# Kernel optimization log

Measured on AMD Instinct MI355X. Metric: run time of the kernel, lower is better.

The kernel has to match this reference:

```python
import jax, jax.numpy as jnp
import numpy as np

_K = 256  # d_model // 8


def setup_inputs() -> dict:
    key = jax.random.key(0)
    ks = jax.random.split(key, 7)
    B, T, D = 4, 4096, 2048
    x = jax.random.normal(ks[0], (B, T, D), jnp.float32)
    ema_mean = 0.1 * jax.random.normal(ks[1], (D,), jnp.float32)
    # ensure positive variance: ema_sq - ema_mean^2 in [0.5, 1.5]
    ema_sq = ema_mean ** 2 + 0.5 + jax.random.uniform(ks[2], (D,), jnp.float32)
    ema_out = jax.random.normal(ks[3], (D,), jnp.float32)
    log_tau = 0.1 * jax.random.normal(ks[4], (), jnp.float32)
    log_sigma_raw = 0.1 * jax.random.normal(ks[5], (), jnp.float32)
    log_w_raw = 0.1 * jax.random.normal(ks[6], (), jnp.float32)
    return {
        "x": x,
        "ema_mean": ema_mean,
        "ema_sq": ema_sq,
        "ema_out": ema_out,
        "log_tau": log_tau,
        "log_sigma_raw": log_sigma_raw,
        "log_w_raw": log_w_raw,
    }


def reference(x, ema_mean, ema_sq, ema_out, log_tau, log_sigma_raw, log_w_raw):
    tau = jnp.exp(log_tau)
    sigma = jax.nn.softplus(log_sigma_raw) + 0.01
    w = jax.nn.softplus(log_w_raw)

    out = jax.nn.gelu(x, approximate=False)  # F.gelu default = exact erf

    # z-score against EMA stats
    std = jnp.sqrt(jnp.clip(ema_sq - ema_mean ** 2, 1e-6, None))
    z = (x - ema_mean) / std

    # topk |z| over channel dim, gather z, mean of |z_topk|
    _, idx = jax.lax.top_k(jnp.abs(z), _K)          # idx: [B,T,K]
    z_topk = jnp.take_along_axis(z, idx, axis=-1)
    topk_mean = jnp.mean(jnp.abs(z_topk), axis=-1, keepdims=True)  # [B,T,1]
    surp = jnp.tanh(sigma * topk_mean)

    # cosine similarity of gelu output against EMA output direction
    ema_u = ema_out / (jnp.linalg.norm(ema_out) + 1e-8)
    out_n = out / jnp.maximum(
        jnp.linalg.norm(out, axis=-1, keepdims=True), 1e-12
    )  # F.normalize eps
    cos_out = jnp.sum(out_n * ema_u, axis=-1, keepdims=True)  # [B,T,1]

    gate = jnp.exp(-tau * cos_out) * (1.0 + w * surp)
    return out * gate
```

## Files before the change

kernel.cpp:

```cpp
#include <hip/hip_runtime.h>
#include <math.h>

#define D      2048
#define KSEL   256
#define NT     256
#define NBINS  256

typedef float vfloat4 __attribute__((ext_vector_type(4)));

__device__ __forceinline__ float fast_gelu(float x) {
    float x2 = x * x;
    float t  = fmaf(x2, -0.0713548162f, -1.5957691216f);
    float e  = __expf(x * t);
    return x * __builtin_amdgcn_rcpf(1.0f + e);
}

__global__ __launch_bounds__(NT) void prep_kernel(
    const float* __restrict__ ema_mean,
    const float* __restrict__ ema_sq,
    const float* __restrict__ ema_out,
    const float* __restrict__ p_log_tau,
    const float* __restrict__ p_log_sigma,
    const float* __restrict__ p_log_w,
    float* __restrict__ ws)
{
    __shared__ float red[4];
    const int tid = threadIdx.x;
    float ss = 0.f;
#pragma unroll
    for (int k = 0; k < D / NT; ++k) {
        int i = tid + k * NT;
        float m = ema_mean[i];
        float v = fmaxf(fmaf(-m, m, ema_sq[i]), 1e-6f);
        float inv = 32.0f * __builtin_amdgcn_rsqf(v);
        ws[i]     = inv;
        ws[D + i] = -m * inv;
        float e = ema_out[i];
        ss = fmaf(e, e, ss);
    }
#pragma unroll
    for (int o = 32; o > 0; o >>= 1) ss += __shfl_down(ss, o, 64);
    if ((tid & 63) == 0) red[tid >> 6] = ss;
    __syncthreads();
    float inv_nrm = 1.0f / (sqrtf(red[0] + red[1] + red[2] + red[3]) + 1e-8f);
#pragma unroll
    for (int k = 0; k < D / NT; ++k) {
        int i = tid + k * NT;
        ws[2 * D + i] = ema_out[i] * inv_nrm;
    }
    if (tid == 0) {
        ws[3 * D + 0] = __expf(p_log_tau[0]);
        ws[3 * D + 1] = __logf(1.0f + __expf(p_log_sigma[0])) + 0.01f;
        ws[3 * D + 2] = __logf(1.0f + __expf(p_log_w[0]));
    }
}

__global__ __launch_bounds__(NT) void row_kernel(
    const float* __restrict__ x,
    const float* __restrict__ ws,
    float* __restrict__ out)
{
    __shared__ int   hist[NBINS];
    __shared__ int   wsum[4];
    __shared__ float red[4][3];
    __shared__ int   bsel_sh, krem_sh;

    const int tid = threadIdx.x;
    const size_t rowoff = (size_t)blockIdx.x * D;
    const float* __restrict__ xr = x + rowoff;

    hist[tid] = 0;

    const float tau   = ws[3 * D + 0];
    const float sigma = ws[3 * D + 1];
    const float w     = ws[3 * D + 2];

    float4 xa = ((const float4*)xr)[tid];
    float4 xb = ((const float4*)xr)[tid + NT];
    float4 aa = ((const float4*)ws)[tid];
    float4 ab = ((const float4*)ws)[tid + NT];
    float4 ba = ((const float4*)(ws + D))[tid];
    float4 bb = ((const float4*)(ws + D))[tid + NT];
    float4 ua = ((const float4*)(ws + 2 * D))[tid];
    float4 ub = ((const float4*)(ws + 2 * D))[tid + NT];

    float xv[8] = {xa.x,xa.y,xa.z,xa.w, xb.x,xb.y,xb.z,xb.w};
    float avv[8] = {aa.x,aa.y,aa.z,aa.w, ab.x,ab.y,ab.z,ab.w};
    float bvv[8] = {ba.x,ba.y,ba.z,ba.w, bb.x,bb.y,bb.z,bb.w};
    float uv[8] = {ua.x,ua.y,ua.z,ua.w, ub.x,ub.y,ub.z,ub.w};

    float g[8], av[8];
    float dot = 0.f, nrm = 0.f;
#pragma unroll
    for (int j = 0; j < 8; ++j) {
        av[j] = fabsf(fmaf(xv[j], avv[j], bvv[j]));
        float gg = fast_gelu(xv[j]);
        g[j] = gg;
        dot = fmaf(gg, uv[j], dot);
        nrm = fmaf(gg, gg, nrm);
    }

    __syncthreads();
#pragma unroll
    for (int j = 0; j < 8; ++j) {
        int b = (int)fminf(av[j], 255.0f);
        atomicAdd(&hist[b], 1);
    }
    __syncthreads();

    {
        int bin = (NBINS - 1) - tid;
        int h = hist[bin];
        int p = h;
#pragma unroll
        for (int o = 1; o < 64; o <<= 1) {
            int t = __shfl_up(p, o, 64);
            if ((tid & 63) >= o) p += t;
        }
        if ((tid & 63) == 63) wsum[tid >> 6] = p;
        __syncthreads();
        int off = 0;
        for (int wv = 0; wv < (tid >> 6); ++wv) off += wsum[wv];
        int suf_incl = p + off;
        int suf_excl = suf_incl - h;
        if (suf_excl < KSEL && suf_incl >= KSEL) {
            bsel_sh = bin;
            krem_sh = KSEL - suf_excl;
        }
    }
    __syncthreads();

    const int   bsel = bsel_sh;
    const float hi  = (bsel == NBINS - 1) ? __builtin_inff() : (float)(bsel + 1);
    const float mid = (float)bsel + 0.5f;

    float s = 0.f;
#pragma unroll
    for (int j = 0; j < 8; ++j) {
        s += (av[j] >= hi) ? av[j] : 0.f;
    }

#pragma unroll
    for (int o = 32; o > 0; o >>= 1) {
        dot += __shfl_down(dot, o, 64);
        nrm += __shfl_down(nrm, o, 64);
        s   += __shfl_down(s,   o, 64);
    }
    const int wave = tid >> 6;
    if ((tid & 63) == 0) {
        red[wave][0] = dot; red[wave][1] = nrm; red[wave][2] = s;
    }
    __syncthreads();
    dot = red[0][0] + red[1][0] + red[2][0] + red[3][0];
    nrm = red[0][1] + red[1][1] + red[2][1] + red[3][1];
    s   = red[0][2] + red[1][2] + red[2][2] + red[3][2];

    const float topk_mean = (s + (float)krem_sh * mid) * (1.0f / (32.0f * KSEL));
    const float cosv = dot * __builtin_amdgcn_rsqf(fmaxf(nrm, 1e-24f));
    const float yt = sigma * topk_mean;
    const float et = __expf(-2.0f * yt);
    const float th = (1.0f - et) * __builtin_amdgcn_rcpf(1.0f + et);
    const float gate = __expf(-tau * cosv) * fmaf(w, th, 1.0f);

    vfloat4 oa, ob;
    oa.x = g[0]*gate; oa.y = g[1]*gate; oa.z = g[2]*gate; oa.w = g[3]*gate;
    ob.x = g[4]*gate; ob.y = g[5]*gate; ob.z = g[6]*gate; ob.w = g[7]*gate;
    vfloat4* outr = (vfloat4*)(out + rowoff);
    __builtin_nontemporal_store(oa, outr + tid);
    __builtin_nontemporal_store(ob, outr + tid + NT);
}

extern "C" void kernel_launch(void* const* d_in, const int* in_sizes, int n_in,
                              void* d_out, int out_size, void* d_ws, size_t ws_size,
                              hipStream_t stream) {
    (void)in_sizes; (void)n_in; (void)out_size; (void)ws_size;
    const float* x         = (const float*)d_in[0];
    const float* ema_mean  = (const float*)d_in[1];
    const float* ema_sq    = (const float*)d_in[2];
    const float* ema_out   = (const float*)d_in[3];
    const float* log_tau   = (const float*)d_in[4];
    const float* log_sigma = (const float*)d_in[5];
    const float* log_w     = (const float*)d_in[6];
    float* out = (float*)d_out;
    float* ws  = (float*)d_ws;

    prep_kernel<<<1, NT, 0, stream>>>(ema_mean, ema_sq, ema_out,
                                      log_tau, log_sigma, log_w, ws);
    const int rows = 4 * 4096;
    row_kernel<<<rows, NT, 0, stream>>>(x, ws, out);
}
```

Measured before the change: 51.71 us.

## Process two rows per 512-thread block and use packed float2 math

Each block now handles two rows with 512 threads, each half keeping its own histogram, scan and reduction buffers, which halves the grid size. The GELU, z-score and dot/norm accumulation are rewritten with two-wide float vectors so the compiler can emit packed FP32 instructions. Block-wide barriers now synchronise both rows together, so the two rows may stall each other. The row count is now taken from the input size.

```diff
diff --git a/kernel.cpp b/kernel.cpp
--- a/kernel.cpp
+++ b/kernel.cpp
@@ -6,14 +6,8 @@
 #define NT     256
 #define NBINS  256
 
-typedef float vfloat4 __attribute__((ext_vector_type(4)));
-
-__device__ __forceinline__ float fast_gelu(float x) {
-    float x2 = x * x;
-    float t  = fmaf(x2, -0.0713548162f, -1.5957691216f);
-    float e  = __expf(x * t);
-    return x * __builtin_amdgcn_rcpf(1.0f + e);
-}
+typedef float f2 __attribute__((ext_vector_type(2)));
+typedef float f4 __attribute__((ext_vector_type(4)));
 
 __global__ __launch_bounds__(NT) void prep_kernel(
     const float* __restrict__ ema_mean,
@@ -55,125 +49,149 @@
     }
 }
 
-__global__ __launch_bounds__(NT) void row_kernel(
+__global__ __launch_bounds__(512) void row_kernel(
     const float* __restrict__ x,
     const float* __restrict__ ws,
     float* __restrict__ out)
 {
-    __shared__ int   hist[NBINS];
-    __shared__ int   wsum[4];
-    __shared__ float red[4][3];
-    __shared__ int   bsel_sh, krem_sh;
-
-    const int tid = threadIdx.x;
-    const size_t rowoff = (size_t)blockIdx.x * D;
+    __shared__ int   hist[2][NBINS];
+    __shared__ int   wsum[2][4];
+    __shared__ float red[2][4][3];
+    __shared__ int   bsel_sh[2], krem_sh[2];
+
+    const int tid  = threadIdx.x;
+    const int half = tid >> 8;
+    const int t    = tid & (NT - 1);
+    const size_t rowoff = ((size_t)blockIdx.x * 2 + half) * (size_t)D;
     const float* __restrict__ xr = x + rowoff;
 
-    hist[tid] = 0;
+    hist[half][t] = 0;
 
     const float tau   = ws[3 * D + 0];
     const float sigma = ws[3 * D + 1];
     const float w     = ws[3 * D + 2];
 
-    float4 xa = ((const float4*)xr)[tid];
-    float4 xb = ((const float4*)xr)[tid + NT];
-    float4 aa = ((const float4*)ws)[tid];
-    float4 ab = ((const float4*)ws)[tid + NT];
-    float4 ba = ((const float4*)(ws + D))[tid];
-    float4 bb = ((const float4*)(ws + D))[tid + NT];
-    float4 ua = ((const float4*)(ws + 2 * D))[tid];
-    float4 ub = ((const float4*)(ws + 2 * D))[tid + NT];
-
-    float xv[8] = {xa.x,xa.y,xa.z,xa.w, xb.x,xb.y,xb.z,xb.w};
-    float avv[8] = {aa.x,aa.y,aa.z,aa.w, ab.x,ab.y,ab.z,ab.w};
-    float bvv[8] = {ba.x,ba.y,ba.z,ba.w, bb.x,bb.y,bb.z,bb.w};
-    float uv[8] = {ua.x,ua.y,ua.z,ua.w, ub.x,ub.y,ub.z,ub.w};
-
-    float g[8], av[8];
-    float dot = 0.f, nrm = 0.f;
+    f4 xa = ((const f4*)xr)[t];
+    f4 xb = ((const f4*)xr)[t + NT];
+    f4 aa = ((const f4*)ws)[t];
+    f4 ab = ((const f4*)ws)[t + NT];
+    f4 ba = ((const f4*)(ws + D))[t];
+    f4 bb = ((const f4*)(ws + D))[t + NT];
+    f4 ua = ((const f4*)(ws + 2 * D))[t];
+    f4 ub = ((const f4*)(ws + 2 * D))[t + NT];
+
+    f2 xp[4] = {xa.lo, xa.hi, xb.lo, xb.hi};
+    f2 ap[4] = {aa.lo, aa.hi, bb.lo, bb.hi};
+    ap[0] = aa.lo; ap[1] = aa.hi; ap[2] = ab.lo; ap[3] = ab.hi;
+    f2 bp[4] = {ba.lo, ba.hi, bb.lo, bb.hi};
+    f2 up[4] = {ua.lo, ua.hi, ub.lo, ub.hi};
+
+    f2 g[4];
+    float av[8];
+    f2 dot2 = (f2)0.f, nrm2 = (f2)0.f;
+#pragma unroll
+    for (int p = 0; p < 4; ++p) {
+        f2 zv = xp[p] * ap[p] + bp[p];
+        av[2 * p]     = zv.x;
+        av[2 * p + 1] = zv.y;
+        f2 x2 = xp[p] * xp[p];
+        f2 tt = x2 * (-0.0713548162f) + (-1.5957691216f);
+        f2 ar = xp[p] * tt;
+        f2 e;
+        e.x = __expf(ar.x);
+        e.y = __expf(ar.y);
+        f2 den = e + 1.0f;
+        f2 r;
+        r.x = __builtin_amdgcn_rcpf(den.x);
+        r.y = __builtin_amdgcn_rcpf(den.y);
+        f2 gg = xp[p] * r;
+        g[p] = gg;
+        dot2 = gg * up[p] + dot2;
+        nrm2 = gg * gg + nrm2;
+    }
+
+    __syncthreads();
 #pragma unroll
     for (int j = 0; j < 8; ++j) {
-        av[j] = fabsf(fmaf(xv[j], avv[j], bvv[j]));
-        float gg = fast_gelu(xv[j]);
-        g[j] = gg;
-        dot = fmaf(gg, uv[j], dot);
-        nrm = fmaf(gg, gg, nrm);
-    }
-
-    __syncthreads();
-#pragma unroll
-    for (int j = 0; j < 8; ++j) {
-        int b = (int)fminf(av[j], 255.0f);
-        atomicAdd(&hist[b], 1);
+        int b = (int)fminf(fabsf(av[j]), 255.0f);
+        atomicAdd(&hist[half][b], 1);
     }
     __syncthreads();
 
     {
-        int bin = (NBINS - 1) - tid;
-        int h = hist[bin];
+        int bin = (NBINS - 1) - t;
+        int h = hist[half][bin];
         int p = h;
 #pragma unroll
         for (int o = 1; o < 64; o <<= 1) {
-            int t = __shfl_up(p, o, 64);
-            if ((tid & 63) >= o) p += t;
+            int q = __shfl_up(p, o, 64);
+            if ((t & 63) >= o) p += q;
         }
-        if ((tid & 63) == 63) wsum[tid >> 6] = p;
+        if ((t & 63) == 63) wsum[half][t >> 6] = p;
         __syncthreads();
         int off = 0;
-        for (int wv = 0; wv < (tid >> 6); ++wv) off += wsum[wv];
+        for (int wv = 0; wv < (t >> 6); ++wv) off += wsum[half][wv];
         int suf_incl = p + off;
         int suf_excl = suf_incl - h;
         if (suf_excl < KSEL && suf_incl >= KSEL) {
-            bsel_sh = bin;
-            krem_sh = KSEL - suf_excl;
+            bsel_sh[half] = bin;
+            krem_sh[half] = KSEL - suf_excl;
         }
     }
     __syncthreads();
 
-    const int   bsel = bsel_sh;
+    const int   bsel = bsel_sh[half];
+    const int   krem = krem_sh[half];
     const float hi  = (bsel == NBINS - 1) ? __builtin_inff() : (float)(bsel + 1);
     const float mid = (float)bsel + 0.5f;
 
     float s = 0.f;
 #pragma unroll
     for (int j = 0; j < 8; ++j) {
-        s += (av[j] >= hi) ? av[j] : 0.f;
-    }
-
+        float a = fabsf(av[j]);
+        s += (a >= hi) ? a : 0.f;
+    }
+
+    float dot = dot2.x + dot2.y;
+    float nrm = nrm2.x + nrm2.y;
 #pragma unroll
     for (int o = 32; o > 0; o >>= 1) {
         dot += __shfl_down(dot, o, 64);
         nrm += __shfl_down(nrm, o, 64);
         s   += __shfl_down(s,   o, 64);
     }
-    const int wave = tid >> 6;
-    if ((tid & 63) == 0) {
-        red[wave][0] = dot; red[wave][1] = nrm; red[wave][2] = s;
-    }
-    __syncthreads();
-    dot = red[0][0] + red[1][0] + red[2][0] + red[3][0];
-    nrm = red[0][1] + red[1][1] + red[2][1] + red[3][1];
-    s   = red[0][2] + red[1][2] + red[2][2] + red[3][2];
-
-    const float topk_mean = (s + (float)krem_sh * mid) * (1.0f / (32.0f * KSEL));
+    const int wave = t >> 6;
+    if ((t & 63) == 0) {
+        red[half][wave][0] = dot;
+        red[half][wave][1] = nrm;
+        red[half][wave][2] = s;
+    }
+    __syncthreads();
+    dot = red[half][0][0] + red[half][1][0] + red[half][2][0] + red[half][3][0];
+    nrm = red[half][0][1] + red[half][1][1] + red[half][2][1] + red[half][3][1];
+    s   = red[half][0][2] + red[half][1][2] + red[half][2][2] + red[half][3][2];
+
+    const float topk_mean = (s + (float)krem * mid) * (1.0f / (32.0f * KSEL));
     const float cosv = dot * __builtin_amdgcn_rsqf(fmaxf(nrm, 1e-24f));
     const float yt = sigma * topk_mean;
     const float et = __expf(-2.0f * yt);
     const float th = (1.0f - et) * __builtin_amdgcn_rcpf(1.0f + et);
     const float gate = __expf(-tau * cosv) * fmaf(w, th, 1.0f);
 
-    vfloat4 oa, ob;
-    oa.x = g[0]*gate; oa.y = g[1]*gate; oa.z = g[2]*gate; oa.w = g[3]*gate;
-    ob.x = g[4]*gate; ob.y = g[5]*gate; ob.z = g[6]*gate; ob.w = g[7]*gate;
-    vfloat4* outr = (vfloat4*)(out + rowoff);
-    __builtin_nontemporal_store(oa, outr + tid);
-    __builtin_nontemporal_store(ob, outr + tid + NT);
+    f4 oa, ob;
+    oa.lo = g[0] * gate;
+    oa.hi = g[1] * gate;
+    ob.lo = g[2] * gate;
+    ob.hi = g[3] * gate;
+    f4* outr = (f4*)(out + rowoff);
+    __builtin_nontemporal_store(oa, outr + t);
+    __builtin_nontemporal_store(ob, outr + t + NT);
 }
 
 extern "C" void kernel_launch(void* const* d_in, const int* in_sizes, int n_in,
                               void* d_out, int out_size, void* d_ws, size_t ws_size,
                               hipStream_t stream) {
-    (void)in_sizes; (void)n_in; (void)out_size; (void)ws_size;
+    (void)n_in; (void)out_size; (void)ws_size;
     const float* x         = (const float*)d_in[0];
     const float* ema_mean  = (const float*)d_in[1];
     const float* ema_sq    = (const float*)d_in[2];
@@ -186,6 +204,6 @@
 
     prep_kernel<<<1, NT, 0, stream>>>(ema_mean, ema_sq, ema_out,
                                       log_tau, log_sigma, log_w, ws);
-    const int rows = 4 * 4096;
-    row_kernel<<<rows, NT, 0, stream>>>(x, ws, out);
+    const int rows = in_sizes[0] / D;
+    row_kernel<<<rows / 2, 512, 0, stream>>>(x, ws, out);
 }
```

Result: slower. 53.37 us (+3.2%).

## Process two rows per block with prefetch and single-wave histogram scan

Applied to the files above, without the earlier changes.

Each block now handles two rows, loading the EMA scale, offset and direction vectors once and prefetching the next row's x while the current row's histogram and reductions run. The 256-bin suffix scan is done by one wave using vectorized int4 reads of the histogram, replacing the block-wide scan and one barrier. The z values are recomputed instead of kept in registers to ease register pressure. Halving the grid reduces parallelism and adds a serial dependency between the two rows inside each block.

```diff
diff --git a/kernel.cpp b/kernel.cpp
--- a/kernel.cpp
+++ b/kernel.cpp
@@ -5,8 +5,10 @@
 #define KSEL   256
 #define NT     256
 #define NBINS  256
-
-typedef float vfloat4 __attribute__((ext_vector_type(4)));
+#define ROWS   2
+
+typedef float f4 __attribute__((ext_vector_type(4)));
+typedef int   i4 __attribute__((ext_vector_type(4)));
 
 __device__ __forceinline__ float fast_gelu(float x) {
     float x2 = x * x;
@@ -61,119 +63,136 @@
     float* __restrict__ out)
 {
     __shared__ int   hist[NBINS];
-    __shared__ int   wsum[4];
     __shared__ float red[4][3];
     __shared__ int   bsel_sh, krem_sh;
 
-    const int tid = threadIdx.x;
-    const size_t rowoff = (size_t)blockIdx.x * D;
-    const float* __restrict__ xr = x + rowoff;
-
-    hist[tid] = 0;
+    const int t    = threadIdx.x;
+    const int wave = t >> 6;
+    const int lane = t & 63;
 
     const float tau   = ws[3 * D + 0];
     const float sigma = ws[3 * D + 1];
     const float w     = ws[3 * D + 2];
 
-    float4 xa = ((const float4*)xr)[tid];
-    float4 xb = ((const float4*)xr)[tid + NT];
-    float4 aa = ((const float4*)ws)[tid];
-    float4 ab = ((const float4*)ws)[tid + NT];
-    float4 ba = ((const float4*)(ws + D))[tid];
-    float4 bb = ((const float4*)(ws + D))[tid + NT];
-    float4 ua = ((const float4*)(ws + 2 * D))[tid];
-    float4 ub = ((const float4*)(ws + 2 * D))[tid + NT];
-
-    float xv[8] = {xa.x,xa.y,xa.z,xa.w, xb.x,xb.y,xb.z,xb.w};
-    float avv[8] = {aa.x,aa.y,aa.z,aa.w, ab.x,ab.y,ab.z,ab.w};
-    float bvv[8] = {ba.x,ba.y,ba.z,ba.w, bb.x,bb.y,bb.z,bb.w};
-    float uv[8] = {ua.x,ua.y,ua.z,ua.w, ub.x,ub.y,ub.z,ub.w};
-
-    float g[8], av[8];
-    float dot = 0.f, nrm = 0.f;
-#pragma unroll
-    for (int j = 0; j < 8; ++j) {
-        av[j] = fabsf(fmaf(xv[j], avv[j], bvv[j]));
-        float gg = fast_gelu(xv[j]);
-        g[j] = gg;
-        dot = fmaf(gg, uv[j], dot);
-        nrm = fmaf(gg, gg, nrm);
-    }
-
+    f4 aa = ((const f4*)ws)[t];
+    f4 ab = ((const f4*)ws)[t + NT];
+    f4 ba = ((const f4*)(ws + D))[t];
+    f4 bb = ((const f4*)(ws + D))[t + NT];
+    f4 ua = ((const f4*)(ws + 2 * D))[t];
+    f4 ub = ((const f4*)(ws + 2 * D))[t + NT];
+    const float a_[8] = {aa.x,aa.y,aa.z,aa.w, ab.x,ab.y,ab.z,ab.w};
+    const float b_[8] = {ba.x,ba.y,ba.z,ba.w, bb.x,bb.y,bb.z,bb.w};
+    const float u_[8] = {ua.x,ua.y,ua.z,ua.w, ub.x,ub.y,ub.z,ub.w};
+
+    const size_t row0 = (size_t)blockIdx.x * ROWS;
+    f4 xa = ((const f4*)(x + row0 * D))[t];
+    f4 xb = ((const f4*)(x + row0 * D))[t + NT];
+
+    hist[t] = 0;
     __syncthreads();
-#pragma unroll
-    for (int j = 0; j < 8; ++j) {
-        int b = (int)fminf(av[j], 255.0f);
-        atomicAdd(&hist[b], 1);
-    }
-    __syncthreads();
-
-    {
-        int bin = (NBINS - 1) - tid;
-        int h = hist[bin];
-        int p = h;
-#pragma unroll
-        for (int o = 1; o < 64; o <<= 1) {
-            int t = __shfl_up(p, o, 64);
-            if ((tid & 63) >= o) p += t;
-        }
-        if ((tid & 63) == 63) wsum[tid >> 6] = p;
+
+#pragma unroll
+    for (int r = 0; r < ROWS; ++r) {
+        const float xv[8] = {xa.x,xa.y,xa.z,xa.w, xb.x,xb.y,xb.z,xb.w};
+
+        float g[8];
+        float dot = 0.f, nrm = 0.f;
+#pragma unroll
+        for (int j = 0; j < 8; ++j) {
+            float gg = fast_gelu(xv[j]);
+            g[j] = gg;
+            dot = fmaf(gg, u_[j], dot);
+            nrm = fmaf(gg, gg, nrm);
+        }
+
+        if (r + 1 < ROWS) {
+            const float* xn = x + (row0 + r + 1) * D;
+            xa = ((const f4*)xn)[t];
+            xb = ((const f4*)xn)[t + NT];
+        }
+
+#pragma unroll
+        for (int j = 0; j < 8; ++j) {
+            float zz = fabsf(fmaf(xv[j], a_[j], b_[j]));
+            int bin = (int)zz;
+            bin = bin > NBINS - 1 ? NBINS - 1 : bin;
+            atomicAdd(&hist[bin], 1);
+        }
         __syncthreads();
-        int off = 0;
-        for (int wv = 0; wv < (tid >> 6); ++wv) off += wsum[wv];
-        int suf_incl = p + off;
-        int suf_excl = suf_incl - h;
-        if (suf_excl < KSEL && suf_incl >= KSEL) {
-            bsel_sh = bin;
-            krem_sh = KSEL - suf_excl;
-        }
-    }
-    __syncthreads();
-
-    const int   bsel = bsel_sh;
-    const float hi  = (bsel == NBINS - 1) ? __builtin_inff() : (float)(bsel + 1);
-    const float mid = (float)bsel + 0.5f;
-
-    float s = 0.f;
-#pragma unroll
-    for (int j = 0; j < 8; ++j) {
-        s += (av[j] >= hi) ? av[j] : 0.f;
-    }
-
-#pragma unroll
-    for (int o = 32; o > 0; o >>= 1) {
-        dot += __shfl_down(dot, o, 64);
-        nrm += __shfl_down(nrm, o, 64);
-        s   += __shfl_down(s,   o, 64);
-    }
-    const int wave = tid >> 6;
-    if ((tid & 63) == 0) {
-        red[wave][0] = dot; red[wave][1] = nrm; red[wave][2] = s;
-    }
-    __syncthreads();
-    dot = red[0][0] + red[1][0] + red[2][0] + red[3][0];
-    nrm = red[0][1] + red[1][1] + red[2][1] + red[3][1];
-    s   = red[0][2] + red[1][2] + red[2][2] + red[3][2];
-
-    const float topk_mean = (s + (float)krem_sh * mid) * (1.0f / (32.0f * KSEL));
-    const float cosv = dot * __builtin_amdgcn_rsqf(fmaxf(nrm, 1e-24f));
-    const float yt = sigma * topk_mean;
-    const float et = __expf(-2.0f * yt);
-    const float th = (1.0f - et) * __builtin_amdgcn_rcpf(1.0f + et);
-    const float gate = __expf(-tau * cosv) * fmaf(w, th, 1.0f);
-
-    vfloat4 oa, ob;
-    oa.x = g[0]*gate; oa.y = g[1]*gate; oa.z = g[2]*gate; oa.w = g[3]*gate;
-    ob.x = g[4]*gate; ob.y = g[5]*gate; ob.z = g[6]*gate; ob.w = g[7]*gate;
-    vfloat4* outr = (vfloat4*)(out + rowoff);
-    __builtin_nontemporal_store(oa, outr + tid);
-    __builtin_nontemporal_store(ob, outr + tid + NT);
+
+        if (wave == 0) {
+            int base = (NBINS - 4) - 4 * lane;
+            i4 v = *(const i4*)&hist[base];
+            int c0 = v.w;
+            int c1 = c0 + v.z;
+            int c2 = c1 + v.y;
+            int c3 = c2 + v.x;
+            int p = c3;
+#pragma unroll
+            for (int o = 1; o < 64; o <<= 1) {
+                int q = __shfl_up(p, o, 64);
+                if (lane >= o) p += q;
+            }
+            int excl = p - c3;
+            int s0 = excl,      i0 = excl + c0;
+            int s1 = i0,        i1 = excl + c1;
+            int s2 = i1,        i2 = excl + c2;
+            int s3 = i2,        i3 = excl + c3;
+            if (s0 < KSEL && i0 >= KSEL) { bsel_sh = base + 3; krem_sh = KSEL - s0; }
+            if (s1 < KSEL && i1 >= KSEL) { bsel_sh = base + 2; krem_sh = KSEL - s1; }
+            if (s2 < KSEL && i2 >= KSEL) { bsel_sh = base + 1; krem_sh = KSEL - s2; }
+            if (s3 < KSEL && i3 >= KSEL) { bsel_sh = base;     krem_sh = KSEL - s3; }
+        }
+        __syncthreads();
+
+        const int   bsel = bsel_sh;
+        const int   krem = krem_sh;
+        const float hi  = (bsel == NBINS - 1) ? __builtin_inff() : (float)(bsel + 1);
+        const float mid = (float)bsel + 0.5f;
+
+        float s = 0.f;
+#pragma unroll
+        for (int j = 0; j < 8; ++j) {
+            float zz = fabsf(fmaf(xv[j], a_[j], b_[j]));
+            s += (zz >= hi) ? zz : 0.f;
+        }
+
+#pragma unroll
+        for (int o = 32; o > 0; o >>= 1) {
+            dot += __shfl_down(dot, o, 64);
+            nrm += __shfl_down(nrm, o, 64);
+            s   += __shfl_down(s,   o, 64);
+        }
+        if (lane == 0) {
+            red[wave][0] = dot; red[wave][1] = nrm; red[wave][2] = s;
+        }
+        hist[t] = 0;
+        __syncthreads();
+
+        dot = red[0][0] + red[1][0] + red[2][0] + red[3][0];
+        nrm = red[0][1] + red[1][1] + red[2][1] + red[3][1];
+        s   = red[0][2] + red[1][2] + red[2][2] + red[3][2];
+
+        const float topk_mean = (s + (float)krem * mid) * (1.0f / (32.0f * KSEL));
+        const float cosv = dot * __builtin_amdgcn_rsqf(fmaxf(nrm, 1e-24f));
+        const float yt = sigma * topk_mean;
+        const float et = __expf(-2.0f * yt);
+        const float th = (1.0f - et) * __builtin_amdgcn_rcpf(1.0f + et);
+        const float gate = __expf(-tau * cosv) * fmaf(w, th, 1.0f);
+
+        f4 oa, ob;
+        oa.x = g[0]*gate; oa.y = g[1]*gate; oa.z = g[2]*gate; oa.w = g[3]*gate;
+        ob.x = g[4]*gate; ob.y = g[5]*gate; ob.z = g[6]*gate; ob.w = g[7]*gate;
+        f4* outr = (f4*)(out + (row0 + r) * D);
+        __builtin_nontemporal_store(oa, outr + t);
+        __builtin_nontemporal_store(ob, outr + t + NT);
+    }
 }
 
 extern "C" void kernel_launch(void* const* d_in, const int* in_sizes, int n_in,
                               void* d_out, int out_size, void* d_ws, size_t ws_size,
                               hipStream_t stream) {
-    (void)in_sizes; (void)n_in; (void)out_size; (void)ws_size;
+    (void)n_in; (void)out_size; (void)ws_size;
     const float* x         = (const float*)d_in[0];
     const float* ema_mean  = (const float*)d_in[1];
     const float* ema_sq    = (const float*)d_in[2];
@@ -186,6 +205,6 @@
 
     prep_kernel<<<1, NT, 0, stream>>>(ema_mean, ema_sq, ema_out,
                                       log_tau, log_sigma, log_w, ws);
-    const int rows = 4 * 4096;
-    row_kernel<<<rows, NT, 0, stream>>>(x, ws, out);
-}
+    const int rows = in_sizes[0] / D;
+    row_kernel<<<rows / ROWS, NT, 0, stream>>>(x, ws, out);
+}
```

Result: faster. 50.29 us (-2.7%).
